# Optimization experiments

Hardware: AMD Instinct MI355X
Metric: run time of the kernel (lower is better)

The kernel has to match this reference:

```python
import jax, jax.numpy as jnp
import numpy as np

N, T = 20000, 32          # vertices, temporal depth
E = 640000                # edges (avg degree 32)
L = 2                     # number of SAGE layers
K, C, PAD = 5, 10, 2      # conv kernel size, out_channels, 'same' padding


def setup_inputs() -> dict:
    key = jax.random.key(0)
    ks = jax.random.split(key, 6)
    x = jax.random.normal(ks[0], (N, T), dtype=jnp.float32)
    edge_index = jax.random.randint(ks[1], (2, E), 0, N)
    # Conv1d(in_channels=1, out_channels=10, kernel_size=5) per layer -> [L, C, 1, K]
    convW = jax.random.normal(ks[2], (L, C, 1, K), dtype=jnp.float32) * 0.3
    convb = jax.random.normal(ks[3], (L, C), dtype=jnp.float32) * 0.1
    # GraphNorm params (initialized as in source: ones/ones/zeros)
    alpha = jnp.ones((L, T), dtype=jnp.float32)
    scale = jnp.ones((L, T), dtype=jnp.float32)
    shift = jnp.zeros((L, T), dtype=jnp.float32)
    # output Linear(in_features=N, out_features=3)
    Wout = jax.random.normal(ks[4], (3, N), dtype=jnp.float32) * (1.0 / np.sqrt(N))
    bout = jax.random.normal(ks[5], (3,), dtype=jnp.float32) * 0.01
    return dict(x=x, convW=convW, convb=convb, alpha=alpha, scale=scale,
                shift=shift, Wout=Wout, bout=bout, edge_index=edge_index)


def reference(x, convW, convb, alpha, scale, shift, Wout, bout, edge_index):
    src = edge_index[0]  # x_j gathered from source nodes
    dst = edge_index[1]  # aggregated at target nodes
    sqrt_n = jnp.sqrt(jnp.asarray(N, x.dtype))
    counts = jax.ops.segment_sum(jnp.ones((E,), x.dtype), dst, num_segments=N)
    denom = jnp.maximum(counts, 1.0)[:, None]  # mean aggr; isolated nodes -> 0
    for l in range(L):
        # GraphNorm
        x = x - alpha[l] * jnp.mean(x, axis=0)
        x = x / (jnp.linalg.norm(x, axis=0) / sqrt_n)
        x = x * scale[l] + shift[l]
        # message: gather + Conv1d(1->10, 'same') + max over channels
        xj = x[src][:, None, :]  # [E, 1, T]
        msg = jax.lax.conv_general_dilated(
            xj, convW[l], window_strides=(1,), padding=[(PAD, PAD)],
            dimension_numbers=('NCH', 'OIH', 'NCH'))  # [E, C, T]
        msg = jnp.max(msg + convb[l][None, :, None], axis=1)  # [E, T]
        # mean scatter-aggregate, then update + ReLU
        aggr = jax.ops.segment_sum(msg, dst, num_segments=N) / denom  # [N, T]
        x = jax.nn.relu(0.5 * (x + aggr))
    s = jnp.sum(x, axis=1)  # [N] sum over temporal dim
    return Wout @ s + bout   # [3] logits
```

## Files before the change

### kernel.cpp

```cpp
#include <hip/hip_runtime.h>
#include <hip/hip_bf16.h>

constexpr int N   = 20000;
constexpr int T   = 32;
constexpr int E   = 640000;
constexpr int C   = 10;
constexpr int K   = 5;
constexpr int SB  = 16;
constexpr int OB  = 64;
constexpr int NR  = 8;
constexpr int CAP = 96;
constexpr int RSPAN  = N / NR;
constexpr int ZWORDS = N + 2 * SB * 64 + OB * 3;

__device__ __forceinline__ float bf_lo(unsigned m) {
    return __uint_as_float(m << 16);
}
__device__ __forceinline__ float bf_hi(unsigned m) {
    return __uint_as_float(m & 0xffff0000u);
}

__global__ void k_zero(int* __restrict__ p) {
    int i = blockIdx.x * 256 + threadIdx.x;
    if (i < ZWORDS) p[i] = 0;
}

__global__ __launch_bounds__(256) void k_bin(
    const int* __restrict__ src, const int* __restrict__ dst,
    int* __restrict__ deg, unsigned short* __restrict__ slot,
    const float* __restrict__ x, float* __restrict__ statsA) {
    __shared__ float sred[64];
    int tid = threadIdx.x;
    int range   = blockIdx.x & (NR - 1);
    int chunk   = blockIdx.x >> 3;
    int nchunks = gridDim.x >> 3;
    int lo = range * RSPAN, hi = lo + RSPAN;
    int per = (E + nchunks - 1) / nchunks;
    int e0 = chunk * per;
    int e1 = e0 + per; if (e1 > E) e1 = E;
    int e = e0 + tid;
    for (; e + 768 < e1; e += 1024) {
        int d0 = dst[e], d1 = dst[e + 256], d2 = dst[e + 512], d3 = dst[e + 768];
        if (d0 >= lo && d0 < hi) {
            int p = atomicAdd(&deg[d0], 1);
            if (p < CAP) slot[d0 * CAP + p] = (unsigned short)src[e];
        }
        if (d1 >= lo && d1 < hi) {
            int p = atomicAdd(&deg[d1], 1);
            if (p < CAP) slot[d1 * CAP + p] = (unsigned short)src[e + 256];
        }
        if (d2 >= lo && d2 < hi) {
            int p = atomicAdd(&deg[d2], 1);
            if (p < CAP) slot[d2 * CAP + p] = (unsigned short)src[e + 512];
        }
        if (d3 >= lo && d3 < hi) {
            int p = atomicAdd(&deg[d3], 1);
            if (p < CAP) slot[d3 * CAP + p] = (unsigned short)src[e + 768];
        }
    }
    for (; e < e1; e += 256) {
        int d = dst[e];
        if (d >= lo && d < hi) {
            int p = atomicAdd(&deg[d], 1);
            if (p < CAP) slot[d * CAP + p] = (unsigned short)src[e];
        }
    }
    int gid = blockIdx.x * 256 + tid;
    int GS  = gridDim.x * 256;
    const float4* x4 = (const float4*)x;
    float s0 = 0.f, s1 = 0.f, s2 = 0.f, s3 = 0.f;
    float q0 = 0.f, q1 = 0.f, q2 = 0.f, q3 = 0.f;
    for (int i = gid; i < N * T / 4; i += GS) {
        float4 v = x4[i];
        s0 += v.x; q0 += v.x * v.x;
        s1 += v.y; q1 += v.y * v.y;
        s2 += v.z; q2 += v.z * v.z;
        s3 += v.w; q3 += v.w * v.w;
    }
    int c4 = (tid & 7) * 4;
#pragma unroll
    for (int ofs = 8; ofs < 64; ofs <<= 1) {
        s0 += __shfl_xor(s0, ofs); q0 += __shfl_xor(q0, ofs);
        s1 += __shfl_xor(s1, ofs); q1 += __shfl_xor(q1, ofs);
        s2 += __shfl_xor(s2, ofs); q2 += __shfl_xor(q2, ofs);
        s3 += __shfl_xor(s3, ofs); q3 += __shfl_xor(q3, ofs);
    }
    if (tid < 64) sred[tid] = 0.f;
    __syncthreads();
    if ((tid & 63) < 8) {
        atomicAdd(&sred[c4 + 0], s0); atomicAdd(&sred[32 + c4 + 0], q0);
        atomicAdd(&sred[c4 + 1], s1); atomicAdd(&sred[32 + c4 + 1], q1);
        atomicAdd(&sred[c4 + 2], s2); atomicAdd(&sred[32 + c4 + 2], q2);
        atomicAdd(&sred[c4 + 3], s3); atomicAdd(&sred[32 + c4 + 3], q3);
    }
    __syncthreads();
    if (tid < 64)
        atomicAdd(&statsA[(blockIdx.x & (SB - 1)) * 64 + tid], sred[tid]);
}

__global__ __launch_bounds__(256) void k_node(
    const float* __restrict__ xin, const float* __restrict__ grep,
    const float* __restrict__ Wl, const float* __restrict__ bl,
    const float* __restrict__ al, const float* __restrict__ sl,
    const float* __restrict__ shl,
    float* __restrict__ xhat, unsigned short* __restrict__ msg) {
    int gid = blockIdx.x * 256 + threadIdx.x;
    int t = gid & 31;
    int row = gid >> 5;
    if (row >= N) return;

    float Sx = 0.f, Sx2 = 0.f;
#pragma unroll
    for (int b = 0; b < SB; ++b) {
        Sx  += grep[b * 64 + t];
        Sx2 += grep[b * 64 + 32 + t];
    }
    float mu   = Sx * (1.0f / (float)N);
    float am   = al[t] * mu;
    float nrm2 = Sx2 - 2.f * am * Sx + (float)N * am * am;
    float g    = sl[t] * sqrtf((float)N) * rsqrtf(nrm2);
    float h    = shl[t] - am * g;

    float v = g * xin[row * T + t] + h;
    xhat[row * T + t] = v;
    float vm2 = __shfl(v, t - 2, 32); if (t < 2)  vm2 = 0.f;
    float vm1 = __shfl(v, t - 1, 32); if (t < 1)  vm1 = 0.f;
    float vp1 = __shfl(v, t + 1, 32); if (t > 30) vp1 = 0.f;
    float vp2 = __shfl(v, t + 2, 32); if (t > 29) vp2 = 0.f;
    float m = -3.0e38f;
#pragma unroll
    for (int c = 0; c < C; ++c) {
        float a = bl[c] + Wl[c * K + 0] * vm2 + Wl[c * K + 1] * vm1
                        + Wl[c * K + 2] * v   + Wl[c * K + 3] * vp1
                        + Wl[c * K + 4] * vp2;
        m = fmaxf(m, a);
    }
    __hip_bfloat16 mb = __float2bfloat16(m);
    msg[row * T + t] = *(unsigned short*)&mb;
}

__device__ __forceinline__ void gather_core(
    const int* __restrict__ deg, const unsigned short* __restrict__ slot,
    const unsigned* __restrict__ msgp, const float* __restrict__ xhat,
    int n, int c, int g, float* v0out, float* v1out) {
    int dg  = deg[n];
    int cnt = dg < CAP ? dg : CAP;
    const unsigned short* sl = slot + n * CAP;
    float a0 = 0.f, a1 = 0.f;
    int i = g;
    for (; i + 12 < cnt; i += 16) {
        int s0 = sl[i], s1 = sl[i + 4], s2 = sl[i + 8], s3 = sl[i + 12];
        unsigned m0 = msgp[s0 * 16 + c];
        unsigned m1 = msgp[s1 * 16 + c];
        unsigned m2 = msgp[s2 * 16 + c];
        unsigned m3 = msgp[s3 * 16 + c];
        a0 += bf_lo(m0); a1 += bf_hi(m0);
        a0 += bf_lo(m1); a1 += bf_hi(m1);
        a0 += bf_lo(m2); a1 += bf_hi(m2);
        a0 += bf_lo(m3); a1 += bf_hi(m3);
    }
    for (; i < cnt; i += 4) {
        unsigned m = msgp[(int)sl[i] * 16 + c];
        a0 += bf_lo(m); a1 += bf_hi(m);
    }
    a0 += __shfl_xor(a0, 16); a0 += __shfl_xor(a0, 32);
    a1 += __shfl_xor(a1, 16); a1 += __shfl_xor(a1, 32);
    float r = 1.0f / fmaxf((float)dg, 1.0f);
    float2 xh = ((const float2*)(xhat + n * T))[c];
    *v0out = fmaxf(0.5f * (xh.x + a0 * r), 0.f);
    *v1out = fmaxf(0.5f * (xh.y + a1 * r), 0.f);
}

__global__ __launch_bounds__(256) void k_gather0(
    const int* __restrict__ deg, const unsigned short* __restrict__ slot,
    const unsigned* __restrict__ msgp, const float* __restrict__ xhat,
    float* __restrict__ xout, float* __restrict__ statsB) {
    __shared__ float sred[64];
    int tid  = threadIdx.x;
    int gid  = blockIdx.x * 256 + tid;
    int lane = tid & 63;
    int g = lane >> 4, c = lane & 15;
    int n = gid >> 6;

    float v0 = 0.f, v1 = 0.f;
    bool valid = (n < N);
    if (valid) {
        gather_core(deg, slot, msgp, xhat, n, c, g, &v0, &v1);
        if (g == 0) {
            float2 w; w.x = v0; w.y = v1;
            ((float2*)(xout + n * T))[c] = w;
        }
    }
    if (tid < 64) sred[tid] = 0.f;
    __syncthreads();
    if (valid && g == 0) {
        atomicAdd(&sred[2 * c],          v0);
        atomicAdd(&sred[2 * c + 1],      v1);
        atomicAdd(&sred[32 + 2 * c],     v0 * v0);
        atomicAdd(&sred[32 + 2 * c + 1], v1 * v1);
    }
    __syncthreads();
    if (tid < 64)
        atomicAdd(&statsB[(blockIdx.x & (SB - 1)) * 64 + tid], sred[tid]);
}

__global__ __launch_bounds__(256) void k_gather1(
    const int* __restrict__ deg, const unsigned short* __restrict__ slot,
    const unsigned* __restrict__ msgp, const float* __restrict__ xhat,
    const float* __restrict__ Wout, float* __restrict__ opart) {
    __shared__ float sred[3];
    int tid  = threadIdx.x;
    int gid  = blockIdx.x * 256 + tid;
    int lane = tid & 63;
    int g = lane >> 4, c = lane & 15;
    int n = gid >> 6;

    float v0 = 0.f, v1 = 0.f;
    bool valid = (n < N);
    if (valid) gather_core(deg, slot, msgp, xhat, n, c, g, &v0, &v1);

    float s = v0 + v1;
    s += __shfl_xor(s, 1); s += __shfl_xor(s, 2);
    s += __shfl_xor(s, 4); s += __shfl_xor(s, 8);
    float pa0 = 0.f, pa1 = 0.f, pa2 = 0.f;
    if (valid && lane == 0) {
        pa0 = Wout[n] * s;
        pa1 = Wout[N + n] * s;
        pa2 = Wout[2 * N + n] * s;
    }
    if (tid < 3) sred[tid] = 0.f;
    __syncthreads();
    if (lane == 0) {
        atomicAdd(&sred[0], pa0);
        atomicAdd(&sred[1], pa1);
        atomicAdd(&sred[2], pa2);
    }
    __syncthreads();
    if (tid < 3)
        atomicAdd(&opart[(blockIdx.x & (OB - 1)) * 3 + tid], sred[tid]);
}

__global__ void k_finout(const float* __restrict__ opart,
                         const float* __restrict__ bout,
                         float* __restrict__ out) {
    int j = threadIdx.x;
    if (j < 3) {
        float s = bout[j];
        for (int b = 0; b < OB; ++b) s += opart[b * 3 + j];
        out[j] = s;
    }
}

extern "C" void kernel_launch(void* const* d_in, const int* in_sizes, int n_in,
                              void* d_out, int out_size, void* d_ws, size_t ws_size,
                              hipStream_t stream) {
    const float* x     = (const float*)d_in[0];
    const float* convW = (const float*)d_in[1];
    const float* convb = (const float*)d_in[2];
    const float* alpha = (const float*)d_in[3];
    const float* scale = (const float*)d_in[4];
    const float* shift = (const float*)d_in[5];
    const float* Wout  = (const float*)d_in[6];
    const float* bout  = (const float*)d_in[7];
    const int*   ei    = (const int*)d_in[8];
    const int* src = ei;
    const int* dst = ei + E;

    int*            deg    = (int*)d_ws;
    float*          statsA = (float*)(deg + N);
    float*          statsB = statsA + SB * 64;
    float*          opart  = statsB + SB * 64;
    unsigned short* slot   = (unsigned short*)(opart + OB * 3);
    unsigned short* msg    = slot + (size_t)N * CAP;
    float*          xhat   = (float*)(msg + (size_t)N * T);
    float*          x1     = xhat + N * T;
    float*          out    = (float*)d_out;

    k_zero<<<(ZWORDS + 255) / 256, 256, 0, stream>>>(deg);

    k_bin<<<2048, 256, 0, stream>>>(src, dst, deg, slot, x, statsA);

    k_node<<<(N * 32 + 255) / 256, 256, 0, stream>>>(
        x, statsA, convW, convb, alpha, scale, shift, xhat, msg);

    k_gather0<<<(N * 64 + 255) / 256, 256, 0, stream>>>(
        deg, slot, (const unsigned*)msg, xhat, x1, statsB);

    k_node<<<(N * 32 + 255) / 256, 256, 0, stream>>>(
        x1, statsB, convW + C * K, convb + C,
        alpha + T, scale + T, shift + T, xhat, msg);

    k_gather1<<<(N * 64 + 255) / 256, 256, 0, stream>>>(
        deg, slot, (const unsigned*)msg, xhat, Wout, opart);

    k_finout<<<1, 64, 0, stream>>>(opart, bout, out);
}
```

Measured before the change: 98.74 us.

## Replace range-filtered edge binning with two-pass shared-memory partition then bin

Edge binning now runs in two kernels. In the first, each edge is read once and bucketed into the 8 destination ranges in shared memory, then written as packed (local dst, src) words to per-block global buffers. In the second, each (range, block) bucket is walked and the degree atomics and slot writes are done. Before, every block re-read its whole dst chunk once per range. This cuts redundant index reads and keeps atomics range-local, at the cost of an extra round trip through global memory and more kernel launches. The x statistics reduction moves into its own kernel, and fixed per-wave and per-block bucket capacities could drop edges if a bucket overflows.

```diff
diff --git a/kernel.cpp b/kernel.cpp
--- a/kernel.cpp
+++ b/kernel.cpp
@@ -10,8 +10,12 @@
 constexpr int OB  = 64;
 constexpr int NR  = 8;
 constexpr int CAP = 96;
-constexpr int RSPAN  = N / NR;
-constexpr int ZWORDS = N + 2 * SB * 64 + OB * 3;
+constexpr int RSPAN = N / NR;
+constexpr int PB   = 625;
+constexpr int PE   = 1024;
+constexpr int WCAP = 80;
+constexpr int PCAP = 320;
+constexpr int ZWORDS = N + 2 * SB * 64 + OB * 3 + NR * PB;
 
 __device__ __forceinline__ float bf_lo(unsigned m) {
     return __uint_as_float(m << 16);
@@ -25,46 +29,66 @@
     if (i < ZWORDS) p[i] = 0;
 }
 
-__global__ __launch_bounds__(256) void k_bin(
+__global__ __launch_bounds__(256) void k_part(
     const int* __restrict__ src, const int* __restrict__ dst,
-    int* __restrict__ deg, unsigned short* __restrict__ slot,
+    unsigned* __restrict__ bufG, int* __restrict__ cnt) {
+    __shared__ unsigned bufL[4][NR][WCAP];
+    __shared__ int cW[4][NR];
+    __shared__ int base[4][NR];
+    int tid = threadIdx.x, w = tid >> 6;
+    if (tid < 32) cW[tid >> 3][tid & 7] = 0;
+    __syncthreads();
+    int e = blockIdx.x * PE + tid * 4;
+    int4 d4 = *(const int4*)(dst + e);
+    int4 s4 = *(const int4*)(src + e);
+    int dd[4] = {d4.x, d4.y, d4.z, d4.w};
+    int ss[4] = {s4.x, s4.y, s4.z, s4.w};
+#pragma unroll
+    for (int k = 0; k < 4; ++k) {
+        int d = dd[k];
+        int r = d / RSPAN;
+        int dl = d - r * RSPAN;
+        int pos = atomicAdd(&cW[w][r], 1);
+        if (pos < WCAP)
+            bufL[w][r][pos] = ((unsigned)dl << 15) | (unsigned)ss[k];
+    }
+    __syncthreads();
+    if (tid < 32) {
+        int ww = tid >> 3, rr = tid & 7;
+        int b = 0;
+        for (int u = 0; u < ww; ++u) b += min(cW[u][rr], WCAP);
+        base[ww][rr] = b;
+        if (ww == 3) cnt[rr * PB + blockIdx.x] = b + min(cW[3][rr], WCAP);
+    }
+    __syncthreads();
+    int lane = tid & 63;
+    for (int r = 0; r < NR; ++r) {
+        int c = min(cW[w][r], WCAP);
+        unsigned* dp = bufG + ((size_t)r * PB + blockIdx.x) * PCAP + base[w][r];
+        for (int i = lane; i < c; i += 64) dp[i] = bufL[w][r][i];
+    }
+}
+
+__global__ __launch_bounds__(64) void k_bin2(
+    const unsigned* __restrict__ bufG, const int* __restrict__ cnt,
+    int* __restrict__ deg, unsigned short* __restrict__ slot) {
+    int r = blockIdx.x & (NR - 1), b = blockIdx.x >> 3;
+    int c = cnt[r * PB + b];
+    const unsigned* bp = bufG + ((size_t)r * PB + b) * PCAP;
+    int lo = r * RSPAN;
+    for (int i = threadIdx.x; i < c; i += 64) {
+        unsigned pk = bp[i];
+        int d = lo + (int)(pk >> 15);
+        int s = (int)(pk & 32767u);
+        int p = atomicAdd(&deg[d], 1);
+        if (p < CAP) slot[d * CAP + p] = (unsigned short)s;
+    }
+}
+
+__global__ __launch_bounds__(256) void k_stats(
     const float* __restrict__ x, float* __restrict__ statsA) {
     __shared__ float sred[64];
     int tid = threadIdx.x;
-    int range   = blockIdx.x & (NR - 1);
-    int chunk   = blockIdx.x >> 3;
-    int nchunks = gridDim.x >> 3;
-    int lo = range * RSPAN, hi = lo + RSPAN;
-    int per = (E + nchunks - 1) / nchunks;
-    int e0 = chunk * per;
-    int e1 = e0 + per; if (e1 > E) e1 = E;
-    int e = e0 + tid;
-    for (; e + 768 < e1; e += 1024) {
-        int d0 = dst[e], d1 = dst[e + 256], d2 = dst[e + 512], d3 = dst[e + 768];
-        if (d0 >= lo && d0 < hi) {
-            int p = atomicAdd(&deg[d0], 1);
-            if (p < CAP) slot[d0 * CAP + p] = (unsigned short)src[e];
-        }
-        if (d1 >= lo && d1 < hi) {
-            int p = atomicAdd(&deg[d1], 1);
-            if (p < CAP) slot[d1 * CAP + p] = (unsigned short)src[e + 256];
-        }
-        if (d2 >= lo && d2 < hi) {
-            int p = atomicAdd(&deg[d2], 1);
-            if (p < CAP) slot[d2 * CAP + p] = (unsigned short)src[e + 512];
-        }
-        if (d3 >= lo && d3 < hi) {
-            int p = atomicAdd(&deg[d3], 1);
-            if (p < CAP) slot[d3 * CAP + p] = (unsigned short)src[e + 768];
-        }
-    }
-    for (; e < e1; e += 256) {
-        int d = dst[e];
-        if (d >= lo && d < hi) {
-            int p = atomicAdd(&deg[d], 1);
-            if (p < CAP) slot[d * CAP + p] = (unsigned short)src[e];
-        }
-    }
     int gid = blockIdx.x * 256 + tid;
     int GS  = gridDim.x * 256;
     const float4* x4 = (const float4*)x;
@@ -270,7 +294,9 @@
     float*          statsA = (float*)(deg + N);
     float*          statsB = statsA + SB * 64;
     float*          opart  = statsB + SB * 64;
-    unsigned short* slot   = (unsigned short*)(opart + OB * 3);
+    int*            cnt    = (int*)(opart + OB * 3);
+    unsigned*       bufG   = (unsigned*)(cnt + NR * PB);
+    unsigned short* slot   = (unsigned short*)(bufG + (size_t)NR * PB * PCAP);
     unsigned short* msg    = slot + (size_t)N * CAP;
     float*          xhat   = (float*)(msg + (size_t)N * T);
     float*          x1     = xhat + N * T;
@@ -278,7 +304,9 @@
 
     k_zero<<<(ZWORDS + 255) / 256, 256, 0, stream>>>(deg);
 
-    k_bin<<<2048, 256, 0, stream>>>(src, dst, deg, slot, x, statsA);
+    k_stats<<<640, 256, 0, stream>>>(x, statsA);
+    k_part<<<PB, 256, 0, stream>>>(src, dst, bufG, cnt);
+    k_bin2<<<NR * PB, 64, 0, stream>>>(bufG, cnt, deg, slot);
 
     k_node<<<(N * 32 + 255) / 256, 256, 0, stream>>>(
         x, statsA, convW, convb, alpha, scale, shift, xhat, msg);
```

After: 99.18 us. No clear change (+0.4%).
